# Optimization experiments

Hardware: AMD Instinct MI355X
Metric: run time of the kernel (lower is better)

The kernel has to match this reference:

```python
import jax, jax.numpy as jnp
import numpy as np
import math
from functools import lru_cache

N_NODES = 30000
N_EDGES = 360000
IN_CH = 256
EDGE_DIM = 64

def parse_irreps(s):
    out = []
    for t in s.split('+'):
        t = t.strip()
        mul, lp = t.split('x')
        out.append((int(mul), int(lp[:-1]), 1 if lp[-1] == 'e' else -1))
    return out

IRR0 = parse_irreps('16x0e')
IRR1 = parse_irreps('16x0e + 2x1o + 2x2e')
IRR2 = parse_irreps('16x0e + 2x1o + 2x1e + 2x2e + 2x2o')
IRR3 = parse_irreps('2x0e + 2x0o + 2x1e + 2x1o + 2x2e + 2x2o + 2x3e + 2x3o')
SH_IRR = parse_irreps('1x0e + 1x1o + 1x2e')

def irreps_dim(irr):
    return sum(m * (2 * l + 1) for m, l, _ in irr)

def instructions(in1, in2, out):
    ins = []
    for i1, (m1, l1, p1) in enumerate(in1):
        for i2, (m2, l2, p2) in enumerate(in2):
            for io, (m3, l3, p3) in enumerate(out):
                if p1 * p2 == p3 and abs(l1 - l2) <= l3 <= l1 + l2:
                    ins.append((i1, i2, io, m1, m2, m3, l1, l2, l3))
    return ins

def weight_numel(in1, in2, out):
    return sum(t[3] * t[4] * t[5] for t in instructions(in1, in2, out))

def _su2_cg(j1, m1, j2, m2, j3, m3):
    if m3 != m1 + m2:
        return 0.0
    f = math.factorial
    vmin = max(-j1 + j2 + m3, -j1 + m1, 0)
    vmax = min(j2 + j3 + m1, j3 - j1 + j2, j3 + m3)
    if vmax < vmin:
        return 0.0
    c = math.sqrt((2 * j3 + 1) * f(j3 + j1 - j2) * f(j3 - j1 + j2) * f(j1 + j2 - j3) * f(j3 + m3) * f(j3 - m3) / (f(j1 + j2 + j3 + 1) * f(j1 - m1) * f(j1 + m1) * f(j2 - m2) * f(j2 + m2)))
    s = 0.0
    for v in range(vmin, vmax + 1):
        s += (-1.0) ** (v + j2 + m2) * f(j2 + j3 + m1 - v) * f(j1 - m1 + v) / (f(v) * f(j3 - j1 + j2 - v) * f(j3 + m3 - v) * f(v + j1 - j2 - m3))
    return c * s

def _q(l):
    q = np.zeros((2 * l + 1, 2 * l + 1), dtype=np.complex128)
    for m in range(-l, 0):
        q[l + m, l + abs(m)] = 2 ** -0.5
        q[l + m, l - abs(m)] = -1j * 2 ** -0.5
    q[l, l] = 1.0
    for m in range(1, l + 1):
        q[l + m, l + abs(m)] = (-1) ** m * 2 ** -0.5
        q[l + m, l - abs(m)] = 1j * (-1) ** m * 2 ** -0.5
    return (-1j) ** l * q

@lru_cache(maxsize=None)
def wigner_3j(l1, l2, l3):
    cg = np.zeros((2 * l1 + 1, 2 * l2 + 1, 2 * l3 + 1), dtype=np.complex128)
    for m1 in range(-l1, l1 + 1):
        for m2 in range(-l2, l2 + 1):
            for m3 in range(-l3, l3 + 1):
                cg[l1 + m1, l2 + m2, l3 + m3] = _su2_cg(l1, m1, l2, m2, l3, m3)
    c = np.einsum('ij,kl,nm,ikn->jlm', _q(l1), _q(l2), np.conj(_q(l3)), cg)
    cr, ci = np.real(c), np.imag(c)
    c = cr if np.linalg.norm(cr) >= np.linalg.norm(ci) else ci
    return jnp.asarray(c / np.linalg.norm(c), dtype=jnp.float32)

def slices(irr):
    offs, o = [], 0
    for m, l, _ in irr:
        offs.append(o)
        o += m * (2 * l + 1)
    return offs

def tensor_product(in1, in2, out, x1, x2, w):
    # e3nn FullyConnectedTensorProduct with external (per-edge) weights
    s1, s2, so = slices(in1), slices(in2), slices(out)
    ins = instructions(in1, in2, out)
    fan = {}
    for _, _, io, m1, m2, _, _, _, _ in ins:
        fan[io] = fan.get(io, 0) + m1 * m2
    e = x1.shape[0]
    res = jnp.zeros((e, irreps_dim(out)), x1.dtype)
    wo = 0
    for i1, i2, io, m1, m2, m3, l1, l2, l3 in ins:
        a = x1[:, s1[i1]:s1[i1] + m1 * (2 * l1 + 1)].reshape(e, m1, 2 * l1 + 1)
        b = x2[:, s2[i2]:s2[i2] + m2 * (2 * l2 + 1)].reshape(e, m2, 2 * l2 + 1)
        nw = m1 * m2 * m3
        ww = w[:, wo:wo + nw].reshape(e, m1, m2, m3)
        wo += nw
        c3 = wigner_3j(l1, l2, l3)
        alpha = math.sqrt((2 * l3 + 1) / fan[io])
        r = alpha * jnp.einsum('ijk,euvw,eui,evj->ewk', c3, ww, a, b)
        res = res.at[:, so[io]:so[io] + m3 * (2 * l3 + 1)].add(r.reshape(e, m3 * (2 * l3 + 1)))
    return res

def sph_harm(vec):
    # '1x0e + 1x1o + 1x2e', normalize=True, 'component' normalization
    n = jnp.sqrt(jnp.sum(vec * vec, axis=-1, keepdims=True))
    u = vec / jnp.maximum(n, 1e-12)
    x, y, z = u[..., 0], u[..., 1], u[..., 2]
    s3, s5, s15 = math.sqrt(3.0), math.sqrt(5.0), math.sqrt(15.0)
    return jnp.stack([jnp.ones_like(x), s3 * y, s3 * z, s3 * x, s15 * x * y, s15 * y * z, 0.5 * s5 * (3 * z * z - 1.0), s15 * x * z, 0.5 * s15 * (x * x - y * y)], axis=-1)

def conv_layer(in_irr, out_irr, node, edge_index, edge_feat, edge_sh, w1, b1, w2, b2, residual):
    src, dst = edge_index[0], edge_index[1]
    w = jax.nn.softplus(edge_feat @ w1 + b1) @ w2 + b2
    tp = tensor_product(in_irr, SH_IRR, out_irr, node[dst], edge_sh, w)
    n = node.shape[0]
    tot = jax.ops.segment_sum(tp, src, num_segments=n)
    cnt = jax.ops.segment_sum(jnp.ones((tp.shape[0],), tp.dtype), src, num_segments=n)
    out = tot / jnp.maximum(cnt, 1.0)[:, None]
    if residual:
        out = out + jnp.pad(node, ((0, 0), (0, out.shape[-1] - node.shape[-1])))
    return out

def _forward(node_feature, edge_vec, edge_feature, edge_index, lin_w, lin_b, f1w1, f1b1, f1w2, f1b2, f2w1, f2b1, f2w2, f2b2, f3w1, f3b1, f3w2, f3b2):
    edge_sh = sph_harm(edge_vec)
    h = node_feature @ lin_w + lin_b
    h = conv_layer(IRR0, IRR1, h, edge_index, edge_feature, edge_sh, f1w1, f1b1, f1w2, f1b2, True)
    h = conv_layer(IRR1, IRR2, h, edge_index, edge_feature, edge_sh, f2w1, f2b1, f2w2, f2b2, False)
    h = conv_layer(IRR2, IRR3, h, edge_index, edge_feature, edge_sh, f3w1, f3b1, f3w2, f3b2, False)
    return h

def setup_inputs() -> dict:
    key = jax.random.key(0)
    ks = jax.random.split(key, 20)
    def rn(k, shape, scale=1.0):
        return scale * jax.random.normal(k, shape, dtype=jnp.float32)
    inp = dict(
        node_feature=rn(ks[0], (N_NODES, IN_CH)),
        edge_vec=rn(ks[1], (N_EDGES, 3)),
        edge_feature=rn(ks[2], (N_EDGES, EDGE_DIM)),
        edge_index=jax.random.randint(ks[3], (2, N_EDGES), 0, N_NODES, dtype=jnp.int32),
        lin_w=rn(ks[4], (IN_CH, 16), IN_CH ** -0.5),
        lin_b=jnp.zeros((16,), jnp.float32),
    )
    wns = [weight_numel(IRR0, SH_IRR, IRR1), weight_numel(IRR1, SH_IRR, IRR2), weight_numel(IRR2, SH_IRR, IRR3)]
    for i, wn in enumerate(wns, 1):
        inp['fc%d_w1' % i] = rn(ks[4 + 4 * i], (EDGE_DIM, EDGE_DIM), EDGE_DIM ** -0.5)
        inp['fc%d_b1' % i] = jnp.zeros((EDGE_DIM,), jnp.float32)
        inp['fc%d_w2' % i] = rn(ks[5 + 4 * i], (EDGE_DIM, wn), EDGE_DIM ** -0.5)
        inp['fc%d_b2' % i] = jnp.zeros((wn,), jnp.float32)
    return inp

def reference(node_feature, edge_vec, edge_feature, edge_index, lin_w, lin_b, fc1_w1, fc1_b1, fc1_w2, fc1_b2, fc2_w1, fc2_b1, fc2_w2, fc2_b2, fc3_w1, fc3_b1, fc3_w2, fc3_b2):
    return _forward(node_feature, edge_vec, edge_feature, edge_index, lin_w, lin_b, fc1_w1, fc1_b1, fc1_w2, fc1_b2, fc2_w1, fc2_b1, fc2_w2, fc2_b2, fc3_w1, fc3_b1, fc3_w2, fc3_b2)
```

## Files before the change

kernel.cpp:

```cpp
#include <hip/hip_runtime.h>
#include <math.h>

#define EDGES 360000
#define NODES 30000
#define NB_SCAN 118

typedef _Float16 h2 __attribute__((ext_vector_type(2)));
typedef _Float16 h8 __attribute__((ext_vector_type(8)));

__device__ inline int imin(int a, int b){ return a < b ? a : b; }
__device__ inline int imax(int a, int b){ return a > b ? a : b; }

__device__ __forceinline__ float fdot2h(h2 a, h2 b, float c){
#if __has_builtin(__builtin_amdgcn_fdot2)
  return __builtin_amdgcn_fdot2(a, b, c, false);
#else
  return c + (float)a[0]*(float)b[0] + (float)a[1]*(float)b[1];
#endif
}

__device__ __forceinline__ float softplusf(float v){
  return fmaxf(v, 0.f) + log1pf(expf(-fabsf(v)));
}


struct cplx { double re, im; };
__device__ inline cplx cmul(cplx a, cplx b){ return { a.re*b.re - a.im*b.im, a.re*b.im + a.im*b.re }; }

__device__ __constant__ double FACT[9] = {1.0,1.0,2.0,6.0,24.0,120.0,720.0,5040.0,40320.0};

__device__ double su2_cg(int j1,int m1,int j2,int m2,int j3,int m3){
  if (m3 != m1 + m2) return 0.0;
  int vmin = imax(imax(-j1 + j2 + m3, -j1 + m1), 0);
  int vmax = imin(imin(j2 + j3 + m1, j3 - j1 + j2), j3 + m3);
  if (vmax < vmin) return 0.0;
  double c = sqrt((2.0*j3 + 1.0) * FACT[j3+j1-j2] * FACT[j3-j1+j2] * FACT[j1+j2-j3]
                  * FACT[j3+m3] * FACT[j3-m3]
                  / (FACT[j1+j2+j3+1] * FACT[j1-m1] * FACT[j1+m1] * FACT[j2-m2] * FACT[j2+m2]));
  double s = 0.0;
  for (int v = vmin; v <= vmax; ++v){
    double t = FACT[j2+j3+m1-v] * FACT[j1-m1+v]
             / (FACT[v] * FACT[j3-j1+j2-v] * FACT[j3+m3-v] * FACT[v+j1-j2-m3]);
    s += (((v + j2 + m2) & 1) ? -t : t);
  }
  return c * s;
}

__device__ cplx qval(int l, int r, int c){
  const double s = 0.7071067811865476;
  int m = r - l;
  cplx v = {0.0, 0.0};
  if (m < 0){
    if      (c == l - m) v = { s, 0.0 };
    else if (c == l + m) v = { 0.0, -s };
  } else if (m == 0){
    if (c == l) v = { 1.0, 0.0 };
  } else {
    double sg = (m & 1) ? -1.0 : 1.0;
    if      (c == l + m) v = { sg*s, 0.0 };
    else if (c == l - m) v = { 0.0, sg*s };
  }
  switch (l & 3){
    case 0: return v;
    case 1: return {  v.im, -v.re };
    case 2: return { -v.re, -v.im };
    default:return { -v.im,  v.re };
  }
}

struct Combo { int l1, l2, l3, off; };
__device__ __constant__ Combo COMBOS[18] = {
  {0,0,0,0},{0,1,1,1},{0,2,2,10},{1,0,1,35},{1,1,0,44},{1,1,1,53},{1,1,2,80},
  {1,2,1,125},{1,2,2,170},{1,2,3,245},{2,0,2,350},{2,1,1,375},{2,1,2,420},
  {2,1,3,495},{2,2,0,600},{2,2,1,625},{2,2,2,700},{2,2,3,825}
};

__global__ void init_cg_kernel(float* __restrict__ cg){
  __shared__ double sr[175], si[175];
  __shared__ double snorm[2];
  const Combo cb = COMBOS[blockIdx.x];
  const int d1 = 2*cb.l1+1, d2 = 2*cb.l2+1, d3 = 2*cb.l3+1;
  const int tot = d1*d2*d3;
  for (int idx = threadIdx.x; idx < tot; idx += blockDim.x){
    int j = idx/(d2*d3), rem = idx - j*(d2*d3);
    int l = rem/d3, m = rem - l*d3;
    double ar = 0.0, ai = 0.0;
    for (int i = 0; i < d1; ++i){
      cplx q1 = qval(cb.l1, i, j);
      if (q1.re == 0.0 && q1.im == 0.0) continue;
      for (int k = 0; k < d2; ++k){
        cplx q2 = qval(cb.l2, k, l);
        if (q2.re == 0.0 && q2.im == 0.0) continue;
        cplx q12 = cmul(q1, q2);
        for (int n = 0; n < d3; ++n){
          double g = su2_cg(cb.l1, i-cb.l1, cb.l2, k-cb.l2, cb.l3, n-cb.l3);
          if (g == 0.0) continue;
          cplx q3 = qval(cb.l3, n, m); q3.im = -q3.im;
          cplx t = cmul(q12, q3);
          ar += t.re * g; ai += t.im * g;
        }
      }
    }
    sr[idx] = ar; si[idx] = ai;
  }
  __syncthreads();
  if (threadIdx.x == 0){
    double nr = 0.0, ni = 0.0;
    for (int t = 0; t < tot; ++t){ nr += sr[t]*sr[t]; ni += si[t]*si[t]; }
    snorm[0] = nr; snorm[1] = ni;
  }
  __syncthreads();
  const bool useR = snorm[0] >= snorm[1];
  const double inv = 1.0 / sqrt(useR ? snorm[0] : snorm[1]);
  for (int idx = threadIdx.x; idx < tot; idx += blockDim.x)
    cg[cb.off + idx] = (float)((useR ? sr[idx] : si[idx]) * inv);
}


struct InsT { int l1,l2,l3,m1,m3,s1,s2,so,woff,cg; float alpha; };

struct L1 {
  static constexpr int NIN = 16, NOUT = 32, WN = 320, NI = 3, NWIN = 3, NU = 16, SROWB = 36;
  static constexpr InsT ins[NI] = {
    {0,0,0,16,16, 0,0, 0,   0,  0, 0.25f},
    {0,1,1,16, 2, 0,1,16, 256,  1, 0.4330127019f},
    {0,2,2,16, 2, 0,4,22, 288, 10, 0.5590169944f},
  };
  static constexpr int uT [NU] = {0,0,0,0,0,0,0,0, 1,1,1,1, 2,2,2,2};
  static constexpr int uCh[NU] = {0,1,2,3,4,5,6,7, 0,1,2,3, 0,1,2,3};
  static constexpr int uD0[NU] = {0,0,0,0,0,0,0,0, 0,0,0,0, 0,0,0,0};
  static constexpr int uND[NU] = {2,2,2,2,2,2,2,2, 4,4,4,4, 4,4,4,4};
  static constexpr int uSl[NU] = {0,1,2,3,0,1,2,3, 0,1,2,3, 0,1,2,3};
};
struct L2 {
  static constexpr int NIN = 32, NOUT = 48, WN = 424, NI = 15, NWIN = 4, NU = 31, SROWB = 68;
  static constexpr InsT ins[NI] = {
    {0,0,0,16,16, 0,0, 0,   0,  0, 0.2236067977f},
    {0,1,1,16, 2, 0,1,16, 256,  1, 0.3692744729f},
    {0,2,2,16, 2, 0,4,28, 288, 10, 0.4767312946f},
    {1,0,1, 2, 2,16,0,16, 320, 35, 0.3692744729f},
    {1,1,0, 2,16,16,1, 0, 324, 44, 0.2236067977f},
    {1,1,1, 2, 2,16,1,22, 356, 53, 0.8660254038f},
    {1,1,2, 2, 2,16,1,28, 360, 80, 0.4767312946f},
    {1,2,1, 2, 2,16,4,16, 364,125, 0.3692744729f},
    {1,2,2, 2, 2,16,4,38, 368,170, 1.1180339887f},
    {2,0,2, 2, 2,22,0,28, 372,350, 0.4767312946f},
    {2,1,1, 2, 2,22,1,16, 376,375, 0.3692744729f},
    {2,1,2, 2, 2,22,1,38, 380,420, 1.1180339887f},
    {2,2,0, 2,16,22,4, 0, 384,600, 0.2236067977f},
    {2,2,1, 2, 2,22,4,22, 416,625, 0.8660254038f},
    {2,2,2, 2, 2,22,4,28, 420,700, 0.4767312946f},
  };
  static constexpr int uT [NU] = {0,0,0,0,0,0,0,0, 1,1,1,1, 2,2,2,2, 3,4,5,6,7,8,9,10,11, 12,12,13,13,14,14};
  static constexpr int uCh[NU] = {0,1,2,3,4,5,6,7, 0,1,2,3, 0,1,2,3, 0,0,0,0,0,0,0,0,0, 0,0,0,0,0,0};
  static constexpr int uD0[NU] = {0,0,0,0,0,0,0,0, 0,0,0,0, 0,0,0,0, 0,0,0,0,0,0,0,0,0, 0,1,0,1,0,1};
  static constexpr int uND[NU] = {2,2,2,2,2,2,2,2, 4,4,4,4, 4,4,4,4, 2,2,2,2,2,2,2,2,2, 1,1,1,1,1,1};
  static constexpr int uSl[NU] = {0,1,2,3,0,1,2,3, 0,1,2,3, 0,1,2,3, 1,0,3,2,2,0,3,3,1, 2,3,2,3,0,1};
};
struct L3 {
  static constexpr int NIN = 48, NOUT = 64, WN = 216, NI = 33, NWIN = 2, NU = 44, SROWB = 100;
  static constexpr InsT ins[NI] = {
    {0,0,0,16,2, 0,0, 0,   0,  0, 0.2236067977f},
    {0,1,1,16,2, 0,1,10,  32,  1, 0.3396831102f},
    {0,2,2,16,2, 0,4,16,  64, 10, 0.4385290097f},
    {1,0,1, 2,2,16,0,10,  96, 35, 0.3396831102f},
    {1,1,0, 2,2,16,1, 0, 100, 44, 0.2236067977f},
    {1,1,1, 2,2,16,1, 4, 104, 53, 0.5477225575f},
    {1,1,2, 2,2,16,1,16, 108, 80, 0.4385290097f},
    {1,2,1, 2,2,16,4,10, 112,125, 0.3396831102f},
    {1,2,2, 2,2,16,4,26, 116,170, 0.7071067812f},
    {1,2,3, 2,2,16,4,50, 120,245, 1.0801234497f},
    {1,0,1, 2,2,22,0, 4, 124, 35, 0.5477225575f},
    {1,1,0, 2,2,22,1, 2, 128, 44, 0.5f},
    {1,1,1, 2,2,22,1,10, 132, 53, 0.3396831102f},
    {1,1,2, 2,2,22,1,26, 136, 80, 0.7071067812f},
    {1,2,1, 2,2,22,4, 4, 140,125, 0.5477225575f},
    {1,2,2, 2,2,22,4,16, 144,170, 0.4385290097f},
    {1,2,3, 2,2,22,4,36, 148,245, 1.0801234497f},
    {2,0,2, 2,2,28,0,16, 152,350, 0.4385290097f},
    {2,1,1, 2,2,28,1,10, 156,375, 0.3396831102f},
    {2,1,2, 2,2,28,1,26, 160,420, 0.7071067812f},
    {2,1,3, 2,2,28,1,50, 164,495, 1.0801234497f},
    {2,2,0, 2,2,28,4, 0, 168,600, 0.2236067977f},
    {2,2,1, 2,2,28,4, 4, 172,625, 0.5477225575f},
    {2,2,2, 2,2,28,4,16, 176,700, 0.4385290097f},
    {2,2,3, 2,2,28,4,36, 180,825, 1.0801234497f},
    {2,0,2, 2,2,38,0,26, 184,350, 0.7071067812f},
    {2,1,1, 2,2,38,1, 4, 188,375, 0.5477225575f},
    {2,1,2, 2,2,38,1,16, 192,420, 0.4385290097f},
    {2,1,3, 2,2,38,1,36, 196,495, 1.0801234497f},
    {2,2,0, 2,2,38,4, 2, 200,600, 0.5f},
    {2,2,1, 2,2,38,4,10, 204,625, 0.3396831102f},
    {2,2,2, 2,2,38,4,26, 208,700, 0.7071067812f},
    {2,2,3, 2,2,38,4,50, 212,825, 1.0801234497f},
  };
  static constexpr int uT [NU] = {0,0,0,0, 1,1,1,1, 2,2,2,2, 3,4,5,6,7,8,9,10,
                                  11,12,13,14,15,16,17,18,19,20,21,22,23, 24,24,
                                  25,26,27,28,29,30,31, 32,32};
  static constexpr int uCh[NU] = {0,1,2,3, 0,1,2,3, 0,1,2,3, 0,0,0,0,0,0,0,0,
                                  0,0,0,0,0,0,0,0,0,0,0,0,0, 0,0,
                                  0,0,0,0,0,0,0, 0,0};
  static constexpr int uD0[NU] = {0,0,0,0, 0,0,0,0, 0,0,0,0, 0,0,0,0,0,0,0,0,
                                  0,0,0,0,0,0,0,0,0,0,0,0,0, 0,1,
                                  0,0,0,0,0,0,0, 0,1};
  static constexpr int uND[NU] = {4,4,4,4, 4,4,4,4, 4,4,4,4, 2,2,2,2,2,2,2,2,
                                  2,2,2,2,2,2,2,2,2,2,2,2,2, 1,1,
                                  2,2,2,2,2,2,2, 1,1};
  static constexpr int uSl[NU] = {0,1,2,3, 3,3,3,3, 0,1,2,3, 2,3,1,2,2,1,0,2,
                                  0,2,3,0,2,0,0,1,2,1,2,3,0, 0,1,
                                  1,3,3,2,3,3,1, 2,3};
};


template<class LD, int SLOT, int WIN, int U>
__device__ __forceinline__ void tp_units(const char* __restrict__ wrow,
    const char* __restrict__ arow, const float* __restrict__ cgs,
    const float (&sh)[9], float (&outv)[LD::NOUT])
{
  if constexpr (U < LD::NU) {
    constexpr int T_ = LD::uT[U];
    constexpr InsT I = LD::ins[T_];
    constexpr int d1 = 2*I.l1+1, d2 = 2*I.l2+1, d3 = 2*I.l3+1;
    constexpr int UCH = (I.m3 == 16) ? 2 : (I.m1 == 16 ? 4 : 2);
    constexpr int NW = UCH * I.m3;
    constexpr int woff_ch = I.woff + LD::uCh[U] * NW;
    if constexpr (LD::uSl[U] == SLOT && woff_ch >= WIN*128 && woff_ch < WIN*128 + 128) {
      constexpr int bl = woff_ch - WIN*128;
      constexpr int D0 = LD::uD0[U];
      constexpr int ND = LD::uND[U];
      #pragma unroll
      for (int dd = 0; dd < ND; ++dd) {
        const int du = D0 + dd;
        const int u  = LD::uCh[U]*UCH + du;
        float ab[d3];
        #pragma unroll
        for (int k = 0; k < d3; ++k) ab[k] = 0.f;
        #pragma unroll
        for (int i = 0; i < d1; ++i) {
          const float ai = (float)*(const _Float16*)(arow + (I.s1 + u*d1 + i)*2);
          #pragma unroll
          for (int j = 0; j < d2; ++j) {
            const float s = ai * sh[I.s2 + j];
            #pragma unroll
            for (int k = 0; k < d3; ++k)
              ab[k] = fmaf(cgs[I.cg + (i*d2 + j)*d3 + k], s, ab[k]);
          }
        }
        #pragma unroll
        for (int wo2 = 0; wo2 < I.m3/2; ++wo2) {
          const h2 wp = *(const h2*)(wrow + (bl + du*I.m3 + 2*wo2)*2);
          const float wv0 = I.alpha * (float)wp[0];
          const float wv1 = I.alpha * (float)wp[1];
          #pragma unroll
          for (int k = 0; k < d3; ++k) {
            outv[I.so + (2*wo2  )*d3 + k] = fmaf(wv0, ab[k], outv[I.so + (2*wo2  )*d3 + k]);
            outv[I.so + (2*wo2+1)*d3 + k] = fmaf(wv1, ab[k], outv[I.so + (2*wo2+1)*d3 + k]);
          }
        }
      }
    }
    tp_units<LD, SLOT, WIN, U+1>(wrow, arow, cgs, sh, outv);
  }
}

template<class LD, int WIN>
__device__ __forceinline__ void tp_win(int slot, const char* wrow, const char* arow,
    const float* cgs, const float (&sh)[9], float (&outv)[LD::NOUT])
{
  switch (slot) {
    case 0: tp_units<LD,0,WIN,0>(wrow, arow, cgs, sh, outv); break;
    case 1: tp_units<LD,1,WIN,0>(wrow, arow, cgs, sh, outv); break;
    case 2: tp_units<LD,2,WIN,0>(wrow, arow, cgs, sh, outv); break;
    default:tp_units<LD,3,WIN,0>(wrow, arow, cgs, sh, outv); break;
  }
}


template<class LD>
__device__ __forceinline__ void stage_w2f(int t, const float* __restrict__ w2,
    char* __restrict__ w2sB, int wbase, int wcols)
{
  const int hh = t >> 5, cc = t & 31;
  if (cc*4 < wcols) {
    #pragma unroll
    for (int r = 0; r < 4; ++r) {
      const int hp = hh + r*8;
      const float4 va = *(const float4*)&w2[(size_t)(2*hp  )*LD::WN + wbase + cc*4];
      const float4 vb = *(const float4*)&w2[(size_t)(2*hp+1)*LD::WN + wbase + cc*4];
      const float a0[4] = {va.x, va.y, va.z, va.w};
      const float b0[4] = {vb.x, vb.y, vb.z, vb.w};
      #pragma unroll
      for (int i = 0; i < 4; ++i) {
        h2 p; p[0] = (_Float16)a0[i]; p[1] = (_Float16)b0[i];
        *(h2*)(w2sB + hp*512 + (cc*4 + i)*4) = p;
      }
    }
  }
}

template<class LD>
__device__ __forceinline__ void fc2f(int t, const float* __restrict__ b2,
    const char* __restrict__ w2sB, const char* __restrict__ hidB,
    char* __restrict__ WsB, int wbase, int wcols)
{
  const int eg = t >> 5, cg = t & 31;
  const int e0 = eg*8, c0 = cg*4;
  if (c0 < wcols) {
    float acc[8][4];
    const float4 bv = *(const float4*)&b2[wbase + c0];
    const float bb[4] = {bv.x, bv.y, bv.z, bv.w};
    #pragma unroll
    for (int ei = 0; ei < 8; ++ei)
      #pragma unroll
      for (int ci = 0; ci < 4; ++ci) acc[ei][ci] = bb[ci];
    for (int hpb = 0; hpb < 8; ++hpb) {
      #pragma unroll
      for (int q = 0; q < 4; ++q) {
        const int hp = hpb*4 + q;
        const h8 wv = *(const h8*)(w2sB + hp*512 + c0*4);
        const h8 ha = *(const h8*)(hidB + hp*272 + e0*4);
        const h8 hb = *(const h8*)(hidB + hp*272 + e0*4 + 16);
        #pragma unroll
        for (int ei = 0; ei < 8; ++ei) {
          const h2 hv = (ei < 4) ? ((const h2*)&ha)[ei] : ((const h2*)&hb)[ei-4];
          #pragma unroll
          for (int ci = 0; ci < 4; ++ci)
            acc[ei][ci] = fdot2h(hv, ((const h2*)&wv)[ci], acc[ei][ci]);
        }
      }
    }
    #pragma unroll
    for (int ei = 0; ei < 8; ++ei) {
      h2 p0, p1;
      p0[0] = (_Float16)acc[ei][0]; p0[1] = (_Float16)acc[ei][1];
      p1[0] = (_Float16)acc[ei][2]; p1[1] = (_Float16)acc[ei][3];
      char* wp = WsB + (e0+ei)*260 + c0*2;
      *(h2*)(wp)     = p0;
      *(h2*)(wp + 4) = p1;
    }
  }
}


template<class LD, int W>
__device__ __forceinline__ void do_windows(int t, int slot,
    const float* __restrict__ b2, const float* __restrict__ w2,
    char* __restrict__ sm, char* __restrict__ hidB, char* __restrict__ w2sB,
    const char* __restrict__ wrow, const char* __restrict__ arow,
    const float* __restrict__ cgs, const float (&sh)[9], float (&outv)[LD::NOUT])
{
  if constexpr (W < LD::NWIN) {
    constexpr int wbase = W*128;
    constexpr int wcols = (LD::WN - wbase < 128) ? (LD::WN - wbase) : 128;
    fc2f<LD>(t, b2, w2sB, hidB, sm, wbase, wcols);
    __syncthreads();
    if constexpr (W + 1 < LD::NWIN) {
      constexpr int nbase = (W+1)*128;
      constexpr int ncols = (LD::WN - nbase < 128) ? (LD::WN - nbase) : 128;
      stage_w2f<LD>(t, w2, w2sB, nbase, ncols);
    }
    tp_win<LD, W>(slot, wrow, arow, cgs, sh, outv);
    __syncthreads();
    do_windows<LD, W+1>(t, slot, b2, w2, sm, hidB, w2sB, wrow, arow, cgs, sh, outv);
  }
}


template<class LD>
__launch_bounds__(256, 3)
__global__ void conv_fused_kernel(const float* __restrict__ node_h,
    const float* __restrict__ edge_vec, const float* __restrict__ edge_feat,
    const int* __restrict__ eidx,
    const float* __restrict__ w1, const float* __restrict__ b1,
    const float* __restrict__ w2, const float* __restrict__ b2,
    const float* __restrict__ cgsrc, float* __restrict__ tp_out)
{
  constexpr int NIN = LD::NIN, NOUT = LD::NOUT;
  constexpr int SROWB = LD::SROWB;
  constexpr int OFF_HIDS = 17408, OFF_W2S = 26112, OFF_AS = 42496;
  constexpr int OFF_CGS = OFF_AS + 64*SROWB;
  static_assert(64*(LD::NOUT + 1)*4 <= OFF_HIDS, "red region too big");
  __shared__ __align__(16) char sm[OFF_CGS + 4000];

  char* efsB = sm;
  char* w1sB = sm + 8704;
  char* hidB = sm + OFF_HIDS;
  char* w2sB = sm + OFF_W2S;
  char* asB  = sm + OFF_AS;
  float* cgs = (float*)(sm + OFF_CGS);

  const int t = threadIdx.x;
  const int e0g = blockIdx.x * 64;

  {
    const float4* efg = (const float4*)edge_feat + (size_t)e0g * 16;
    #pragma unroll
    for (int r = 0; r < 4; ++r) {
      const int f = r*256 + t;
      const float4 v = efg[f];
      const int e = f >> 4, c0 = (f & 15) * 4;
      h2 pa; pa[0] = (_Float16)v.x; pa[1] = (_Float16)v.y;
      h2 pb; pb[0] = (_Float16)v.z; pb[1] = (_Float16)v.w;
      *(h2*)(efsB + (c0>>1)*272 + e*4)     = pa;
      *(h2*)(efsB + ((c0>>1)+1)*272 + e*4) = pb;
    }
    const int cp = t >> 3, hq = t & 7, hb = hq*8;
    const float4 wa0 = *(const float4*)&w1[(size_t)(2*cp)*64 + hb];
    const float4 wa1 = *(const float4*)&w1[(size_t)(2*cp)*64 + hb + 4];
    const float4 wb0 = *(const float4*)&w1[(size_t)(2*cp+1)*64 + hb];
    const float4 wb1 = *(const float4*)&w1[(size_t)(2*cp+1)*64 + hb + 4];
    const float a0[8] = {wa0.x,wa0.y,wa0.z,wa0.w, wa1.x,wa1.y,wa1.z,wa1.w};
    const float b0[8] = {wb0.x,wb0.y,wb0.z,wb0.w, wb1.x,wb1.y,wb1.z,wb1.w};
    #pragma unroll
    for (int i = 0; i < 8; ++i) {
      h2 p; p[0] = (_Float16)a0[i]; p[1] = (_Float16)b0[i];
      *(h2*)(w1sB + cp*272 + (hb+i)*4) = p;
    }
    for (int i = t; i < 64*NIN; i += 256) {
      const int e = i / NIN, c = i - e*NIN;
      const int dst = eidx[EDGES + e0g + e];
      *(_Float16*)(asB + e*SROWB + c*2) = (_Float16)node_h[(size_t)dst*NIN + c];
    }
    for (int i = t; i < 1000; i += 256) cgs[i] = cgsrc[i];
    stage_w2f<LD>(t, w2, w2sB, 0, (LD::WN < 128) ? LD::WN : 128);
  }
  __syncthreads();

  {
    const int hg = t >> 4, eg2 = t & 15;
    const int h0 = hg*4, e0 = eg2*4;
    float acc[4][4];
    const float4 b1v = *(const float4*)&b1[h0];
    const float bb[4] = {b1v.x, b1v.y, b1v.z, b1v.w};
    #pragma unroll
    for (int j = 0; j < 4; ++j)
      #pragma unroll
      for (int i = 0; i < 4; ++i) acc[j][i] = bb[j];
    #pragma unroll 4
    for (int cp = 0; cp < 32; ++cp) {
      const h8 ev = *(const h8*)(efsB + cp*272 + e0*4);
      const h8 wv = *(const h8*)(w1sB + cp*272 + h0*4);
      #pragma unroll
      for (int j = 0; j < 4; ++j)
        #pragma unroll
        for (int i = 0; i < 4; ++i)
          acc[j][i] = fdot2h(((const h2*)&wv)[j], ((const h2*)&ev)[i], acc[j][i]);
    }
    #pragma unroll
    for (int i = 0; i < 4; ++i) {
      #pragma unroll
      for (int jp = 0; jp < 2; ++jp) {
        h2 p;
        p[0] = (_Float16)softplusf(acc[2*jp  ][i]);
        p[1] = (_Float16)softplusf(acc[2*jp+1][i]);
        *(h2*)(hidB + (2*hg + jp)*272 + (e0+i)*4) = p;
      }
    }
  }

  const int slot = t >> 6;
  const int le = t & 63;
  const int eme = e0g + le;
  float sh[9];
  {
    const float vx = edge_vec[(size_t)eme*3 + 0];
    const float vy = edge_vec[(size_t)eme*3 + 1];
    const float vz = edge_vec[(size_t)eme*3 + 2];
    const float nrm = sqrtf(vx*vx + vy*vy + vz*vz);
    const float invn = 1.0f / fmaxf(nrm, 1e-12f);
    const float x = vx*invn, y = vy*invn, z = vz*invn;
    sh[0] = 1.0f;
    sh[1] = 1.7320508076f * y;
    sh[2] = 1.7320508076f * z;
    sh[3] = 1.7320508076f * x;
    sh[4] = 3.8729833462f * x * y;
    sh[5] = 3.8729833462f * y * z;
    sh[6] = 1.1180339887f * (3.0f*z*z - 1.0f);
    sh[7] = 3.8729833462f * x * z;
    sh[8] = 1.9364916731f * (x*x - y*y);
  }
  float outv[NOUT];
  #pragma unroll
  for (int o = 0; o < NOUT; ++o) outv[o] = 0.f;
  const char* wrow = sm + le * 260;
  const char* arow = asB + le * SROWB;
  __syncthreads();

  do_windows<LD, 0>(t, slot, b2, w2, sm, hidB, w2sB, wrow, arow, cgs, sh, outv);

  constexpr int PAD = NOUT + 1;
  float* red = (float*)sm;
  float* myrow = red + (size_t)le * PAD;
  if (slot == 3) {
    #pragma unroll
    for (int o = 0; o < NOUT; ++o) myrow[o] = outv[o];
  }
  __syncthreads();
  if (slot == 2) {
    #pragma unroll
    for (int o = 0; o < NOUT; ++o) myrow[o] += outv[o];
  }
  __syncthreads();
  if (slot == 1) {
    #pragma unroll
    for (int o = 0; o < NOUT; ++o) myrow[o] += outv[o];
  }
  __syncthreads();
  if (slot == 0) {
    float* dst = tp_out + (size_t)eme * NOUT;
    #pragma unroll
    for (int o = 0; o < NOUT; o += 4) {
      float4 v;
      v.x = myrow[o]   + outv[o];
      v.y = myrow[o+1] + outv[o+1];
      v.z = myrow[o+2] + outv[o+2];
      v.w = myrow[o+3] + outv[o+3];
      *(float4*)&dst[o] = v;
    }
  }
}


__global__ void cnt_kernel(const int* __restrict__ eidx, int* __restrict__ cnti){
  const int e = blockIdx.x * 256 + threadIdx.x;
  if (e < EDGES) atomicAdd(&cnti[eidx[e]], 1);
}

__global__ void scanA_kernel(const int* __restrict__ cnti, int* __restrict__ escan,
                             int* __restrict__ bsum){
  __shared__ int s[256];
  const int t = threadIdx.x, idx = blockIdx.x*256 + t;
  int v = (idx < NODES) ? cnti[idx] : 0;
  s[t] = v; __syncthreads();
  for (int off = 1; off < 256; off <<= 1){
    int x = (t >= off) ? s[t-off] : 0;
    __syncthreads();
    s[t] += x;
    __syncthreads();
  }
  if (idx < NODES) escan[idx] = s[t];
  if (t == 255) bsum[blockIdx.x] = s[255];
}

__global__ void scanB_kernel(const int* __restrict__ bsum, int* __restrict__ boff){
  __shared__ int s[128];
  const int t = threadIdx.x;
  int v = (t < NB_SCAN) ? bsum[t] : 0;
  s[t] = v; __syncthreads();
  for (int off = 1; off < 128; off <<= 1){
    int x = (t >= off) ? s[t-off] : 0;
    __syncthreads();
    s[t] += x;
    __syncthreads();
  }
  if (t < NB_SCAN) boff[t] = s[t] - v;
}

__global__ void scanC_kernel(const int* __restrict__ escan, const int* __restrict__ cnti,
                             const int* __restrict__ boff, int* __restrict__ eoff,
                             int* __restrict__ ecur){
  const int idx = blockIdx.x*256 + threadIdx.x;
  if (idx < NODES){
    const int v = escan[idx] - cnti[idx] + boff[blockIdx.x];
    eoff[idx] = v; ecur[idx] = v;
  }
  if (idx == 0) eoff[NODES] = EDGES;
}

__global__ void fill_eids_kernel(const int* __restrict__ eidx, int* __restrict__ ecur,
                                 int* __restrict__ eids){
  const int e = blockIdx.x * 256 + threadIdx.x;
  if (e < EDGES){
    const int p = atomicAdd(&ecur[eidx[e]], 1);
    eids[p] = e;
  }
}


template<int NOUT, bool RES>
__global__ void gather_kernel(const float* __restrict__ tp_out,
    const int* __restrict__ eoff, const int* __restrict__ eids,
    const float* __restrict__ h0, float* __restrict__ out)
{
  const int node = blockIdx.x * 4 + (threadIdx.x >> 6);
  const int lane = threadIdx.x & 63;
  if (node >= NODES) return;
  const int s = eoff[node], e_end = eoff[node+1];
  if (lane < NOUT) {
    float v = 0.f;
    for (int k = s; k < e_end; ++k) {
      const int e = eids[k];
      v += tp_out[(size_t)e*NOUT + lane];
    }
    v /= fmaxf((float)(e_end - s), 1.0f);
    if (RES && lane < 16) v += h0[node*16 + lane];
    out[(size_t)node*NOUT + lane] = v;
  }
}


__global__ void lin_kernel(const float* __restrict__ nf, const float* __restrict__ w,
                           const float* __restrict__ b, float* __restrict__ h0){
  const int idx = blockIdx.x * 256 + threadIdx.x;
  if (idx >= NODES * 16) return;
  const int n = idx >> 4, o = idx & 15;
  const float* __restrict__ row = nf + (size_t)n * 256;
  float acc = b[o];
  for (int c = 0; c < 256; ++c) acc = fmaf(row[c], w[c*16 + o], acc);
  h0[idx] = acc;
}


extern "C" void kernel_launch(void* const* d_in, const int* in_sizes, int n_in,
                              void* d_out, int out_size, void* d_ws, size_t ws_size,
                              hipStream_t stream) {
  (void)in_sizes; (void)n_in; (void)out_size; (void)ws_size;
  const float* node_feature = (const float*)d_in[0];
  const float* edge_vec     = (const float*)d_in[1];
  const float* edge_feature = (const float*)d_in[2];
  const int*   edge_index   = (const int*)d_in[3];
  const float* lin_w = (const float*)d_in[4];
  const float* lin_b = (const float*)d_in[5];
  const float* f1w1 = (const float*)d_in[6];
  const float* f1b1 = (const float*)d_in[7];
  const float* f1w2 = (const float*)d_in[8];
  const float* f1b2 = (const float*)d_in[9];
  const float* f2w1 = (const float*)d_in[10];
  const float* f2b1 = (const float*)d_in[11];
  const float* f2w2 = (const float*)d_in[12];
  const float* f2b2 = (const float*)d_in[13];
  const float* f3w1 = (const float*)d_in[14];
  const float* f3b1 = (const float*)d_in[15];
  const float* f3w2 = (const float*)d_in[16];
  const float* f3b2 = (const float*)d_in[17];

  float* ws   = (float*)d_ws;
  float* cg   = ws;
  int*   cnti = (int*)(ws + 1024);
  int*   escan= (int*)(ws + 32768);
  int*   bsum = (int*)(ws + 65536);
  int*   boff = (int*)(ws + 65792);
  int*   eoff = (int*)(ws + 66048);
  int*   ecur = (int*)(ws + 98304);
  int*   eids = (int*)(ws + 131072);
  float* h0   = ws + 524288;
  float* h1   = ws + 1048576;
  float* h2p  = ws + 2097152;
  float* tpo  = ws + 3538944;
  float* outp = (float*)d_out;

  (void)hipMemsetAsync(cnti, 0, NODES * sizeof(int), stream);

  init_cg_kernel<<<18, 256, 0, stream>>>(cg);
  cnt_kernel<<<(EDGES + 255)/256, 256, 0, stream>>>(edge_index, cnti);
  scanA_kernel<<<NB_SCAN, 256, 0, stream>>>(cnti, escan, bsum);
  scanB_kernel<<<1, 128, 0, stream>>>(bsum, boff);
  scanC_kernel<<<NB_SCAN, 256, 0, stream>>>(escan, cnti, boff, eoff, ecur);
  fill_eids_kernel<<<(EDGES + 255)/256, 256, 0, stream>>>(edge_index, ecur, eids);
  lin_kernel<<<(NODES*16 + 255)/256, 256, 0, stream>>>(node_feature, lin_w, lin_b, h0);

  const int egrid = EDGES / 64;
  const int ggrid = (NODES + 3) / 4;

  conv_fused_kernel<L1><<<egrid, 256, 0, stream>>>(h0, edge_vec, edge_feature, edge_index,
                                                   f1w1, f1b1, f1w2, f1b2, cg, tpo);
  gather_kernel<32, true><<<ggrid, 256, 0, stream>>>(tpo, eoff, eids, h0, h1);

  conv_fused_kernel<L2><<<egrid, 256, 0, stream>>>(h1, edge_vec, edge_feature, edge_index,
                                                   f2w1, f2b1, f2w2, f2b2, cg, tpo);
  gather_kernel<48, false><<<ggrid, 256, 0, stream>>>(tpo, eoff, eids, h0, h2p);

  conv_fused_kernel<L3><<<egrid, 256, 0, stream>>>(h2p, edge_vec, edge_feature, edge_index,
                                                   f3w1, f3b1, f3w2, f3b2, cg, tpo);
  gather_kernel<64, false><<<ggrid, 256, 0, stream>>>(tpo, eoff, eids, h0, outp);
}
```

Baseline: 1.599 ms.

## Process 128 edges per block with one thread per edge for tensor product

Each block now handles 128 edges instead of 64. Only the first 128 threads run the tensor product, one edge per thread, with node features held in registers. The old scheme split each edge's units across four slots and summed them through shared memory, and that reduction is removed. FC2 windows shrink to 64 columns with a new LDS layout and new thread tiling, and w1 is read straight from global memory instead of being staged. The price is half the threads sitting idle during the tensor-product phase, more windows and barriers, and lower occupancy (launch bounds 2).

```diff
diff --git a/kernel.cpp b/kernel.cpp
--- a/kernel.cpp
+++ b/kernel.cpp
@@ -4,6 +4,7 @@
 #define EDGES 360000
 #define NODES 30000
 #define NB_SCAN 118
+#define EPB 128
 
 typedef _Float16 h2 __attribute__((ext_vector_type(2)));
 typedef _Float16 h8 __attribute__((ext_vector_type(8)));
@@ -120,7 +121,7 @@
 struct InsT { int l1,l2,l3,m1,m3,s1,s2,so,woff,cg; float alpha; };
 
 struct L1 {
-  static constexpr int NIN = 16, NOUT = 32, WN = 320, NI = 3, NWIN = 3, NU = 16, SROWB = 36;
+  static constexpr int NIN = 16, NOUT = 32, WN = 320, NI = 3, NWIN = 5, NU = 16;
   static constexpr InsT ins[NI] = {
     {0,0,0,16,16, 0,0, 0,   0,  0, 0.25f},
     {0,1,1,16, 2, 0,1,16, 256,  1, 0.4330127019f},
@@ -130,10 +131,9 @@
   static constexpr int uCh[NU] = {0,1,2,3,4,5,6,7, 0,1,2,3, 0,1,2,3};
   static constexpr int uD0[NU] = {0,0,0,0,0,0,0,0, 0,0,0,0, 0,0,0,0};
   static constexpr int uND[NU] = {2,2,2,2,2,2,2,2, 4,4,4,4, 4,4,4,4};
-  static constexpr int uSl[NU] = {0,1,2,3,0,1,2,3, 0,1,2,3, 0,1,2,3};
 };
 struct L2 {
-  static constexpr int NIN = 32, NOUT = 48, WN = 424, NI = 15, NWIN = 4, NU = 31, SROWB = 68;
+  static constexpr int NIN = 32, NOUT = 48, WN = 424, NI = 15, NWIN = 7, NU = 30;
   static constexpr InsT ins[NI] = {
     {0,0,0,16,16, 0,0, 0,   0,  0, 0.2236067977f},
     {0,1,1,16, 2, 0,1,16, 256,  1, 0.3692744729f},
@@ -151,14 +151,13 @@
     {2,2,1, 2, 2,22,4,22, 416,625, 0.8660254038f},
     {2,2,2, 2, 2,22,4,28, 420,700, 0.4767312946f},
   };
-  static constexpr int uT [NU] = {0,0,0,0,0,0,0,0, 1,1,1,1, 2,2,2,2, 3,4,5,6,7,8,9,10,11, 12,12,13,13,14,14};
-  static constexpr int uCh[NU] = {0,1,2,3,4,5,6,7, 0,1,2,3, 0,1,2,3, 0,0,0,0,0,0,0,0,0, 0,0,0,0,0,0};
-  static constexpr int uD0[NU] = {0,0,0,0,0,0,0,0, 0,0,0,0, 0,0,0,0, 0,0,0,0,0,0,0,0,0, 0,1,0,1,0,1};
-  static constexpr int uND[NU] = {2,2,2,2,2,2,2,2, 4,4,4,4, 4,4,4,4, 2,2,2,2,2,2,2,2,2, 1,1,1,1,1,1};
-  static constexpr int uSl[NU] = {0,1,2,3,0,1,2,3, 0,1,2,3, 0,1,2,3, 1,0,3,2,2,0,3,3,1, 2,3,2,3,0,1};
+  static constexpr int uT [NU] = {0,0,0,0,0,0,0,0, 1,1,1,1, 2,2,2,2, 3, 4,4, 5, 6,7,8, 9,10,11, 12,12, 13,14};
+  static constexpr int uCh[NU] = {0,1,2,3,4,5,6,7, 0,1,2,3, 0,1,2,3, 0, 0,0, 0, 0,0,0, 0,0,0, 0,0, 0,0};
+  static constexpr int uD0[NU] = {0,0,0,0,0,0,0,0, 0,0,0,0, 0,0,0,0, 0, 0,1, 0, 0,0,0, 0,0,0, 0,1, 0,0};
+  static constexpr int uND[NU] = {2,2,2,2,2,2,2,2, 4,4,4,4, 4,4,4,4, 2, 1,1, 2, 2,2,2, 2,2,2, 1,1, 2,2};
 };
 struct L3 {
-  static constexpr int NIN = 48, NOUT = 64, WN = 216, NI = 33, NWIN = 2, NU = 44, SROWB = 100;
+  static constexpr int NIN = 48, NOUT = 64, WN = 216, NI = 33, NWIN = 4, NU = 42;
   static constexpr InsT ins[NI] = {
     {0,0,0,16,2, 0,0, 0,   0,  0, 0.2236067977f},
     {0,1,1,16,2, 0,1,10,  32,  1, 0.3396831102f},
@@ -194,38 +193,46 @@
     {2,2,2, 2,2,38,4,26, 208,700, 0.7071067812f},
     {2,2,3, 2,2,38,4,50, 212,825, 1.0801234497f},
   };
-  static constexpr int uT [NU] = {0,0,0,0, 1,1,1,1, 2,2,2,2, 3,4,5,6,7,8,9,10,
-                                  11,12,13,14,15,16,17,18,19,20,21,22,23, 24,24,
-                                  25,26,27,28,29,30,31, 32,32};
-  static constexpr int uCh[NU] = {0,1,2,3, 0,1,2,3, 0,1,2,3, 0,0,0,0,0,0,0,0,
-                                  0,0,0,0,0,0,0,0,0,0,0,0,0, 0,0,
-                                  0,0,0,0,0,0,0, 0,0};
-  static constexpr int uD0[NU] = {0,0,0,0, 0,0,0,0, 0,0,0,0, 0,0,0,0,0,0,0,0,
-                                  0,0,0,0,0,0,0,0,0,0,0,0,0, 0,1,
-                                  0,0,0,0,0,0,0, 0,1};
-  static constexpr int uND[NU] = {4,4,4,4, 4,4,4,4, 4,4,4,4, 2,2,2,2,2,2,2,2,
-                                  2,2,2,2,2,2,2,2,2,2,2,2,2, 1,1,
-                                  2,2,2,2,2,2,2, 1,1};
-  static constexpr int uSl[NU] = {0,1,2,3, 3,3,3,3, 0,1,2,3, 2,3,1,2,2,1,0,2,
-                                  0,2,3,0,2,0,0,1,2,1,2,3,0, 0,1,
-                                  1,3,3,2,3,3,1, 2,3};
+  static constexpr int uT [NU] = {0,0,0,0, 1,1,1,1, 2,2,2,2,
+    3,4,5,6,7,8,9,10,11,12,13,14,15,16,17,18,19,20,21,22,23,24,25,26,27,28,29,30,31,32};
+  static constexpr int uCh[NU] = {0,1,2,3, 0,1,2,3, 0,1,2,3,
+    0,0,0,0,0,0,0,0,0,0,0,0,0,0,0,0,0,0,0,0,0,0,0,0,0,0,0,0,0,0};
+  static constexpr int uD0[NU] = {0,0,0,0, 0,0,0,0, 0,0,0,0,
+    0,0,0,0,0,0,0,0,0,0,0,0,0,0,0,0,0,0,0,0,0,0,0,0,0,0,0,0,0,0};
+  static constexpr int uND[NU] = {4,4,4,4, 4,4,4,4, 4,4,4,4,
+    2,2,2,2,2,2,2,2,2,2,2,2,2,2,2,2,2,2,2,2,2,2,2,2,2,2,2,2,2,2};
 };
 
-
-template<class LD, int SLOT, int WIN, int U>
-__device__ __forceinline__ void tp_units(const char* __restrict__ wrow,
-    const char* __restrict__ arow, const float* __restrict__ cgs,
+template<class LD>
+constexpr int colsum(){
+  int s = 0;
+  for (int u = 0; u < LD::NU; ++u) s += LD::uND[u] * LD::ins[LD::uT[u]].m3;
+  return s;
+}
+static_assert(colsum<L1>() == L1::WN, "L1 col coverage");
+static_assert(colsum<L2>() == L2::WN, "L2 col coverage");
+static_assert(colsum<L3>() == L3::WN, "L3 col coverage");
+
+#define OFF_WREG 16896
+#define OFF_CGS  34304
+#define OFF_W2S  38304
+#define SM_BYTES 47008
+static_assert(SM_BYTES < 65536, "static LDS must be < 64KB");
+
+
+template<class LD, int WIN, int U>
+__device__ __forceinline__ void tp_units(const char* wrow,
+    const float (&a)[LD::NIN], const float* __restrict__ cgs,
     const float (&sh)[9], float (&outv)[LD::NOUT])
 {
   if constexpr (U < LD::NU) {
-    constexpr int T_ = LD::uT[U];
-    constexpr InsT I = LD::ins[T_];
+    constexpr InsT I = LD::ins[LD::uT[U]];
     constexpr int d1 = 2*I.l1+1, d2 = 2*I.l2+1, d3 = 2*I.l3+1;
     constexpr int UCH = (I.m3 == 16) ? 2 : (I.m1 == 16 ? 4 : 2);
     constexpr int NW = UCH * I.m3;
     constexpr int woff_ch = I.woff + LD::uCh[U] * NW;
-    if constexpr (LD::uSl[U] == SLOT && woff_ch >= WIN*128 && woff_ch < WIN*128 + 128) {
-      constexpr int bl = woff_ch - WIN*128;
+    if constexpr (woff_ch >= WIN*64 && woff_ch < WIN*64 + 64) {
+      constexpr int bl = woff_ch - WIN*64;
       constexpr int D0 = LD::uD0[U];
       constexpr int ND = LD::uND[U];
       #pragma unroll
@@ -237,7 +244,7 @@
         for (int k = 0; k < d3; ++k) ab[k] = 0.f;
         #pragma unroll
         for (int i = 0; i < d1; ++i) {
-          const float ai = (float)*(const _Float16*)(arow + (I.s1 + u*d1 + i)*2);
+          const float ai = a[I.s1 + u*d1 + i];
           #pragma unroll
           for (int j = 0; j < d2; ++j) {
             const float s = ai * sh[I.s2 + j];
@@ -259,19 +266,7 @@
         }
       }
     }
-    tp_units<LD, SLOT, WIN, U+1>(wrow, arow, cgs, sh, outv);
-  }
-}
-
-template<class LD, int WIN>
-__device__ __forceinline__ void tp_win(int slot, const char* wrow, const char* arow,
-    const float* cgs, const float (&sh)[9], float (&outv)[LD::NOUT])
-{
-  switch (slot) {
-    case 0: tp_units<LD,0,WIN,0>(wrow, arow, cgs, sh, outv); break;
-    case 1: tp_units<LD,1,WIN,0>(wrow, arow, cgs, sh, outv); break;
-    case 2: tp_units<LD,2,WIN,0>(wrow, arow, cgs, sh, outv); break;
-    default:tp_units<LD,3,WIN,0>(wrow, arow, cgs, sh, outv); break;
+    tp_units<LD, WIN, U+1>(wrow, a, cgs, sh, outv);
   }
 }
 
@@ -280,11 +275,11 @@
 __device__ __forceinline__ void stage_w2f(int t, const float* __restrict__ w2,
     char* __restrict__ w2sB, int wbase, int wcols)
 {
-  const int hh = t >> 5, cc = t & 31;
+  const int hh = t >> 4, cc = t & 15;
   if (cc*4 < wcols) {
     #pragma unroll
-    for (int r = 0; r < 4; ++r) {
-      const int hp = hh + r*8;
+    for (int r = 0; r < 2; ++r) {
+      const int hp = hh + r*16;
       const float4 va = *(const float4*)&w2[(size_t)(2*hp  )*LD::WN + wbase + cc*4];
       const float4 vb = *(const float4*)&w2[(size_t)(2*hp+1)*LD::WN + wbase + cc*4];
       const float a0[4] = {va.x, va.y, va.z, va.w};
@@ -292,7 +287,7 @@
       #pragma unroll
       for (int i = 0; i < 4; ++i) {
         h2 p; p[0] = (_Float16)a0[i]; p[1] = (_Float16)b0[i];
-        *(h2*)(w2sB + hp*512 + (cc*4 + i)*4) = p;
+        *(h2*)(w2sB + hp*272 + (cc*4 + i)*4) = p;
       }
     }
   }
@@ -301,73 +296,73 @@
 template<class LD>
 __device__ __forceinline__ void fc2f(int t, const float* __restrict__ b2,
     const char* __restrict__ w2sB, const char* __restrict__ hidB,
-    char* __restrict__ WsB, int wbase, int wcols)
+    char* Wreg, int wbase, int wcols)
 {
-  const int eg = t >> 5, cg = t & 31;
-  const int e0 = eg*8, c0 = cg*4;
+  const int eg = t >> 3, cg = t & 7;
+  const int e0 = eg*4, c0 = cg*8;
   if (c0 < wcols) {
-    float acc[8][4];
-    const float4 bv = *(const float4*)&b2[wbase + c0];
-    const float bb[4] = {bv.x, bv.y, bv.z, bv.w};
-    #pragma unroll
-    for (int ei = 0; ei < 8; ++ei)
-      #pragma unroll
-      for (int ci = 0; ci < 4; ++ci) acc[ei][ci] = bb[ci];
-    for (int hpb = 0; hpb < 8; ++hpb) {
-      #pragma unroll
-      for (int q = 0; q < 4; ++q) {
-        const int hp = hpb*4 + q;
-        const h8 wv = *(const h8*)(w2sB + hp*512 + c0*4);
-        const h8 ha = *(const h8*)(hidB + hp*272 + e0*4);
-        const h8 hb = *(const h8*)(hidB + hp*272 + e0*4 + 16);
+    float acc[4][8];
+    const float4 bv0 = *(const float4*)&b2[wbase + c0];
+    const float4 bv1 = *(const float4*)&b2[wbase + c0 + 4];
+    const float bb[8] = {bv0.x,bv0.y,bv0.z,bv0.w, bv1.x,bv1.y,bv1.z,bv1.w};
+    #pragma unroll
+    for (int ei = 0; ei < 4; ++ei)
+      #pragma unroll
+      for (int ci = 0; ci < 8; ++ci) acc[ei][ci] = bb[ci];
+    for (int hp = 0; hp < 32; ++hp) {
+      const h8 wv0 = *(const h8*)(w2sB + hp*272 + c0*4);
+      const h8 wv1 = *(const h8*)(w2sB + hp*272 + c0*4 + 16);
+      const h8 hv  = *(const h8*)(hidB + hp*528 + e0*4);
+      #pragma unroll
+      for (int ei = 0; ei < 4; ++ei) {
+        const h2 hve = ((const h2*)&hv)[ei];
         #pragma unroll
-        for (int ei = 0; ei < 8; ++ei) {
-          const h2 hv = (ei < 4) ? ((const h2*)&ha)[ei] : ((const h2*)&hb)[ei-4];
-          #pragma unroll
-          for (int ci = 0; ci < 4; ++ci)
-            acc[ei][ci] = fdot2h(hv, ((const h2*)&wv)[ci], acc[ei][ci]);
+        for (int ci = 0; ci < 8; ++ci) {
+          const h2 wv = (ci < 4) ? ((const h2*)&wv0)[ci] : ((const h2*)&wv1)[ci-4];
+          acc[ei][ci] = fdot2h(hve, wv, acc[ei][ci]);
         }
       }
     }
     #pragma unroll
-    for (int ei = 0; ei < 8; ++ei) {
-      h2 p0, p1;
-      p0[0] = (_Float16)acc[ei][0]; p0[1] = (_Float16)acc[ei][1];
-      p1[0] = (_Float16)acc[ei][2]; p1[1] = (_Float16)acc[ei][3];
-      char* wp = WsB + (e0+ei)*260 + c0*2;
-      *(h2*)(wp)     = p0;
-      *(h2*)(wp + 4) = p1;
+    for (int ei = 0; ei < 4; ++ei) {
+      char* wp = Wreg + (e0+ei)*136 + c0*2;
+      #pragma unroll
+      for (int ci = 0; ci < 4; ++ci) {
+        h2 p; p[0] = (_Float16)acc[ei][2*ci]; p[1] = (_Float16)acc[ei][2*ci+1];
+        *(h2*)(wp + ci*4) = p;
+      }
     }
   }
 }
 
 
 template<class LD, int W>
-__device__ __forceinline__ void do_windows(int t, int slot,
+__device__ __forceinline__ void do_windows(int t,
     const float* __restrict__ b2, const float* __restrict__ w2,
-    char* __restrict__ sm, char* __restrict__ hidB, char* __restrict__ w2sB,
-    const char* __restrict__ wrow, const char* __restrict__ arow,
+    char* Wreg, char* __restrict__ hidB, char* __restrict__ w2sB,
+    const char* wrow, const float (&a)[LD::NIN],
     const float* __restrict__ cgs, const float (&sh)[9], float (&outv)[LD::NOUT])
 {
   if constexpr (W < LD::NWIN) {
-    constexpr int wbase = W*128;
-    constexpr int wcols = (LD::WN - wbase < 128) ? (LD::WN - wbase) : 128;
-    fc2f<LD>(t, b2, w2sB, hidB, sm, wbase, wcols);
+    constexpr int wbase = W*64;
+    constexpr int wcols = (LD::WN - wbase < 64) ? (LD::WN - wbase) : 64;
+    fc2f<LD>(t, b2, w2sB, hidB, Wreg, wbase, wcols);
     __syncthreads();
     if constexpr (W + 1 < LD::NWIN) {
-      constexpr int nbase = (W+1)*128;
-      constexpr int ncols = (LD::WN - nbase < 128) ? (LD::WN - nbase) : 128;
+      constexpr int nbase = (W+1)*64;
+      constexpr int ncols = (LD::WN - nbase < 64) ? (LD::WN - nbase) : 64;
       stage_w2f<LD>(t, w2, w2sB, nbase, ncols);
     }
-    tp_win<LD, W>(slot, wrow, arow, cgs, sh, outv);
+    if (t < EPB)
+      tp_units<LD, W, 0>(wrow, a, cgs, sh, outv);
     __syncthreads();
-    do_windows<LD, W+1>(t, slot, b2, w2, sm, hidB, w2sB, wrow, arow, cgs, sh, outv);
+    do_windows<LD, W+1>(t, b2, w2, Wreg, hidB, w2sB, wrow, a, cgs, sh, outv);
   }
 }
 
 
 template<class LD>
-__launch_bounds__(256, 3)
+__launch_bounds__(256, 2)
 __global__ void conv_fused_kernel(const float* __restrict__ node_h,
     const float* __restrict__ edge_vec, const float* __restrict__ edge_feat,
     const int* __restrict__ eidx,
@@ -376,96 +371,92 @@
     const float* __restrict__ cgsrc, float* __restrict__ tp_out)
 {
   constexpr int NIN = LD::NIN, NOUT = LD::NOUT;
-  constexpr int SROWB = LD::SROWB;
-  constexpr int OFF_HIDS = 17408, OFF_W2S = 26112, OFF_AS = 42496;
-  constexpr int OFF_CGS = OFF_AS + 64*SROWB;
-  static_assert(64*(LD::NOUT + 1)*4 <= OFF_HIDS, "red region too big");
-  __shared__ __align__(16) char sm[OFF_CGS + 4000];
-
-  char* efsB = sm;
-  char* w1sB = sm + 8704;
-  char* hidB = sm + OFF_HIDS;
+  __shared__ __align__(16) char sm[SM_BYTES];
+  char* hidB = sm;
+  char* Wreg = sm + OFF_WREG;
+  char* efsB = sm + OFF_WREG;
+  float* cgs = (float*)(sm + OFF_CGS);
   char* w2sB = sm + OFF_W2S;
-  char* asB  = sm + OFF_AS;
-  float* cgs = (float*)(sm + OFF_CGS);
 
   const int t = threadIdx.x;
-  const int e0g = blockIdx.x * 64;
+  const int e0g = blockIdx.x * EPB;
 
   {
     const float4* efg = (const float4*)edge_feat + (size_t)e0g * 16;
     #pragma unroll
-    for (int r = 0; r < 4; ++r) {
+    for (int r = 0; r < 8; ++r) {
       const int f = r*256 + t;
-      const float4 v = efg[f];
       const int e = f >> 4, c0 = (f & 15) * 4;
+      float4 v = make_float4(0.f, 0.f, 0.f, 0.f);
+      if (e0g + e < EDGES) v = efg[f];
       h2 pa; pa[0] = (_Float16)v.x; pa[1] = (_Float16)v.y;
       h2 pb; pb[0] = (_Float16)v.z; pb[1] = (_Float16)v.w;
-      *(h2*)(efsB + (c0>>1)*272 + e*4)     = pa;
-      *(h2*)(efsB + ((c0>>1)+1)*272 + e*4) = pb;
-    }
-    const int cp = t >> 3, hq = t & 7, hb = hq*8;
-    const float4 wa0 = *(const float4*)&w1[(size_t)(2*cp)*64 + hb];
-    const float4 wa1 = *(const float4*)&w1[(size_t)(2*cp)*64 + hb + 4];
-    const float4 wb0 = *(const float4*)&w1[(size_t)(2*cp+1)*64 + hb];
-    const float4 wb1 = *(const float4*)&w1[(size_t)(2*cp+1)*64 + hb + 4];
-    const float a0[8] = {wa0.x,wa0.y,wa0.z,wa0.w, wa1.x,wa1.y,wa1.z,wa1.w};
-    const float b0[8] = {wb0.x,wb0.y,wb0.z,wb0.w, wb1.x,wb1.y,wb1.z,wb1.w};
-    #pragma unroll
-    for (int i = 0; i < 8; ++i) {
-      h2 p; p[0] = (_Float16)a0[i]; p[1] = (_Float16)b0[i];
-      *(h2*)(w1sB + cp*272 + (hb+i)*4) = p;
-    }
-    for (int i = t; i < 64*NIN; i += 256) {
-      const int e = i / NIN, c = i - e*NIN;
-      const int dst = eidx[EDGES + e0g + e];
-      *(_Float16*)(asB + e*SROWB + c*2) = (_Float16)node_h[(size_t)dst*NIN + c];
+      *(h2*)(efsB + (c0>>1)*528 + e*4)     = pa;
+      *(h2*)(efsB + ((c0>>1)+1)*528 + e*4) = pb;
     }
     for (int i = t; i < 1000; i += 256) cgs[i] = cgsrc[i];
-    stage_w2f<LD>(t, w2, w2sB, 0, (LD::WN < 128) ? LD::WN : 128);
+    stage_w2f<LD>(t, w2, w2sB, 0, (LD::WN < 64) ? LD::WN : 64);
   }
   __syncthreads();
 
   {
     const int hg = t >> 4, eg2 = t & 15;
-    const int h0 = hg*4, e0 = eg2*4;
-    float acc[4][4];
+    const int h0 = hg*4, e0 = eg2*8;
+    float acc[4][8];
     const float4 b1v = *(const float4*)&b1[h0];
     const float bb[4] = {b1v.x, b1v.y, b1v.z, b1v.w};
     #pragma unroll
     for (int j = 0; j < 4; ++j)
       #pragma unroll
-      for (int i = 0; i < 4; ++i) acc[j][i] = bb[j];
-    #pragma unroll 4
+      for (int i = 0; i < 8; ++i) acc[j][i] = bb[j];
     for (int cp = 0; cp < 32; ++cp) {
-      const h8 ev = *(const h8*)(efsB + cp*272 + e0*4);
-      const h8 wv = *(const h8*)(w1sB + cp*272 + h0*4);
-      #pragma unroll
-      for (int j = 0; j < 4; ++j)
+      const float4 w1a = *(const float4*)&w1[(size_t)(2*cp)*64 + h0];
+      const float4 w1b = *(const float4*)&w1[(size_t)(2*cp+1)*64 + h0];
+      h2 wp[4];
+      wp[0][0]=(_Float16)w1a.x; wp[0][1]=(_Float16)w1b.x;
+      wp[1][0]=(_Float16)w1a.y; wp[1][1]=(_Float16)w1b.y;
+      wp[2][0]=(_Float16)w1a.z; wp[2][1]=(_Float16)w1b.z;
+      wp[3][0]=(_Float16)w1a.w; wp[3][1]=(_Float16)w1b.w;
+      #pragma unroll
+      for (int q = 0; q < 2; ++q) {
+        const h8 ev = *(const h8*)(efsB + cp*528 + (e0 + q*4)*4);
         #pragma unroll
-        for (int i = 0; i < 4; ++i)
-          acc[j][i] = fdot2h(((const h2*)&wv)[j], ((const h2*)&ev)[i], acc[j][i]);
-    }
-    #pragma unroll
-    for (int i = 0; i < 4; ++i) {
+        for (int j = 0; j < 4; ++j)
+          #pragma unroll
+          for (int i = 0; i < 4; ++i)
+            acc[j][q*4 + i] = fdot2h(wp[j], ((const h2*)&ev)[i], acc[j][q*4 + i]);
+      }
+    }
+    #pragma unroll
+    for (int i = 0; i < 8; ++i) {
       #pragma unroll
       for (int jp = 0; jp < 2; ++jp) {
         h2 p;
         p[0] = (_Float16)softplusf(acc[2*jp  ][i]);
         p[1] = (_Float16)softplusf(acc[2*jp+1][i]);
-        *(h2*)(hidB + (2*hg + jp)*272 + (e0+i)*4) = p;
+        *(h2*)(hidB + (2*hg + jp)*528 + (e0+i)*4) = p;
       }
     }
   }
 
-  const int slot = t >> 6;
-  const int le = t & 63;
-  const int eme = e0g + le;
+  const int tl  = imin(t, EPB - 1);
+  const int eme = e0g + t;
+  const int emc = imin(e0g + tl, EDGES - 1);
+  const int dst = eidx[EDGES + emc];
+  float a[NIN];
+  {
+    const float4* av = (const float4*)(node_h + (size_t)dst * NIN);
+    #pragma unroll
+    for (int i = 0; i < NIN/4; ++i) {
+      const float4 q = av[i];
+      a[4*i+0] = q.x; a[4*i+1] = q.y; a[4*i+2] = q.z; a[4*i+3] = q.w;
+    }
+  }
   float sh[9];
   {
-    const float vx = edge_vec[(size_t)eme*3 + 0];
-    const float vy = edge_vec[(size_t)eme*3 + 1];
-    const float vz = edge_vec[(size_t)eme*3 + 2];
+    const float vx = edge_vec[(size_t)emc*3 + 0];
+    const float vy = edge_vec[(size_t)emc*3 + 1];
+    const float vz = edge_vec[(size_t)emc*3 + 2];
     const float nrm = sqrtf(vx*vx + vy*vy + vz*vz);
     const float invn = 1.0f / fmaxf(nrm, 1e-12f);
     const float x = vx*invn, y = vy*invn, z = vz*invn;
@@ -482,40 +473,17 @@
   float outv[NOUT];
   #pragma unroll
   for (int o = 0; o < NOUT; ++o) outv[o] = 0.f;
-  const char* wrow = sm + le * 260;
-  const char* arow = asB + le * SROWB;
+  const char* wrow = Wreg + tl * 136;
   __syncthreads();
 
-  do_windows<LD, 0>(t, slot, b2, w2, sm, hidB, w2sB, wrow, arow, cgs, sh, outv);
-
-  constexpr int PAD = NOUT + 1;
-  float* red = (float*)sm;
-  float* myrow = red + (size_t)le * PAD;
-  if (slot == 3) {
-    #pragma unroll
-    for (int o = 0; o < NOUT; ++o) myrow[o] = outv[o];
-  }
-  __syncthreads();
-  if (slot == 2) {
-    #pragma unroll
-    for (int o = 0; o < NOUT; ++o) myrow[o] += outv[o];
-  }
-  __syncthreads();
-  if (slot == 1) {
-    #pragma unroll
-    for (int o = 0; o < NOUT; ++o) myrow[o] += outv[o];
-  }
-  __syncthreads();
-  if (slot == 0) {
-    float* dst = tp_out + (size_t)eme * NOUT;
+  do_windows<LD, 0>(t, b2, w2, Wreg, hidB, w2sB, wrow, a, cgs, sh, outv);
+
+  if (t < EPB && eme < EDGES) {
+    float* dstp = tp_out + (size_t)eme * NOUT;
     #pragma unroll
     for (int o = 0; o < NOUT; o += 4) {
-      float4 v;
-      v.x = myrow[o]   + outv[o];
-      v.y = myrow[o+1] + outv[o+1];
-      v.z = myrow[o+2] + outv[o+2];
-      v.w = myrow[o+3] + outv[o+3];
-      *(float4*)&dst[o] = v;
+      float4 v = {outv[o], outv[o+1], outv[o+2], outv[o+3]};
+      *(float4*)&dstp[o] = v;
     }
   }
 }
@@ -659,7 +627,7 @@
   fill_eids_kernel<<<(EDGES + 255)/256, 256, 0, stream>>>(edge_index, ecur, eids);
   lin_kernel<<<(NODES*16 + 255)/256, 256, 0, stream>>>(node_feature, lin_w, lin_b, h0);
 
-  const int egrid = EDGES / 64;
+  const int egrid = (EDGES + EPB - 1) / EPB;
   const int ggrid = (NODES + 3) / 4;
 
   conv_fused_kernel<L1><<<egrid, 256, 0, stream>>>(h0, edge_vec, edge_feature, edge_index,
```

Result: slower. 1.835 ms (+14.7%).
